# Kernel tuning notes

Measured on AMD Instinct MI355X. Metric: run time of the kernel, lower is better.

The kernel has to match this reference:

```python
import jax, jax.numpy as jnp
import numpy as np

N = 16        # state dim n
M = 8         # control dim m
T = 50        # time_steps
DT = 0.01     # delta_t
SQRT_DT = DT ** 0.5
GAMMA = 0.1
SIGMA = 0.2
TAU = 0.5
H = 10        # hidden width of subnets
BATCH = 32768


def _mlp(params, x):
    W1, b1, W2, b2, W3, b3 = params
    h = jnp.tanh(x @ W1 + b1)
    h = jnp.tanh(h @ W2 + b2)
    return h @ W3 + b3


def setup_inputs() -> dict:
    key = jax.random.key(0)
    ks = jax.random.split(key, 32)

    def dense(k, i, o):
        return (jax.random.normal(k, (i, o), jnp.float32) / np.float32(np.sqrt(i)))

    inp = {
        'dw': jax.random.normal(ks[0], (T, BATCH, 1), jnp.float32) * SQRT_DT,
        'X0': jax.random.uniform(ks[1], (BATCH, N), jnp.float32),
        'A': dense(ks[2], N, N),
        'Bmat': dense(ks[3], N, M),
        'Cmat': dense(ks[4], N, N),
        'Dmat': dense(ks[5], N, M),
        # phi: (n+1) -> 10 -> 10 -> m
        'phi_W1': dense(ks[6], N + 1, H), 'phi_b1': jnp.zeros((H,), jnp.float32),
        'phi_W2': dense(ks[7], H, H),     'phi_b2': jnp.zeros((H,), jnp.float32),
        'phi_W3': dense(ks[8], H, M),     'phi_b3': jnp.zeros((M,), jnp.float32),
        # Z: (n+1) -> 10 -> 10 -> n
        'Z_W1': dense(ks[9], N + 1, H),   'Z_b1': jnp.zeros((H,), jnp.float32),
        'Z_W2': dense(ks[10], H, H),      'Z_b2': jnp.zeros((H,), jnp.float32),
        'Z_W3': dense(ks[11], H, N),      'Z_b3': jnp.zeros((N,), jnp.float32),
        # Y0: n -> 10 -> 10 -> n
        'Y0_W1': dense(ks[12], N, H),     'Y0_b1': jnp.zeros((H,), jnp.float32),
        'Y0_W2': dense(ks[13], H, H),     'Y0_b2': jnp.zeros((H,), jnp.float32),
        'Y0_W3': dense(ks[14], H, N),     'Y0_b3': jnp.zeros((N,), jnp.float32),
    }
    return inp


def reference(dw, X0, A, Bmat, Cmat, Dmat,
              phi_W1, phi_b1, phi_W2, phi_b2, phi_W3, phi_b3,
              Z_W1, Z_b1, Z_W2, Z_b2, Z_W3, Z_b3,
              Y0_W1, Y0_b1, Y0_W2, Y0_b2, Y0_W3, Y0_b3):
    phi_p = (phi_W1, phi_b1, phi_W2, phi_b2, phi_W3, phi_b3)
    Z_p = (Z_W1, Z_b1, Z_W2, Z_b2, Z_W3, Z_b3)
    Y0_p = (Y0_W1, Y0_b1, Y0_W2, Y0_b2, Y0_W3, Y0_b3)

    B = X0.shape[0]
    Y = _mlp(Y0_p, X0)                              # [B, n]
    t_grid = jnp.arange(T, dtype=X0.dtype) * DT     # [T]
    w_trap = jnp.ones((T,), X0.dtype).at[1:-1].set(2.0)  # trapezoid weights

    def step(carry, xs):
        X, Yc, lc = carry
        dwi, t, w = xs                              # dwi: [B,1]
        state = jnp.concatenate(
            [jnp.broadcast_to(t, (B, 1)).astype(X.dtype), X], axis=1)  # [B, n+1]
        Zv = _mlp(Z_p, state)                       # [B, n]
        u = _mlp(phi_p, state)                      # [B, m] (project = identity)
        # b_mult(M, x) == x @ M.T
        drift_X = X @ A.T + u @ Bmat.T + GAMMA      # [B, n]
        diffusion_X = X @ Cmat.T + u @ Dmat.T + SIGMA
        drift_Y = -(Yc @ A + Zv @ Cmat + X)         # f_x(X,u) = X
        # stop_recording branch: gradient of dH / pre_phi
        dH = Yc @ Bmat + Zv @ Dmat + u              # f_u(X,u) = u -> [B, m]
        pre_phi = jax.lax.stop_gradient(u - TAU * dH)
        Xn = X + drift_X * DT + dwi * diffusion_X
        Yn = Yc + drift_Y * DT + dwi * Zv
        lc = lc + 0.5 * DT * w * jnp.sum(jnp.square(u - pre_phi), axis=1)
        return (Xn, Yn, lc), None

    init = (X0, Y, jnp.zeros((B,), X0.dtype))
    (X, Y, loss_control), _ = jax.lax.scan(step, init, (dw, t_grid, w_trap))
    loss_bsde = jnp.sum(jnp.square(Y - X), axis=1)  # g_x(X) = X
    return jnp.stack([jnp.mean(loss_bsde), jnp.mean(loss_control)])
```

## Files before the change

kernel.cpp:

```cpp
#include <hip/hip_runtime.h>

namespace {

typedef float v4f __attribute__((ext_vector_type(4)));
typedef _Float16 half4 __attribute__((ext_vector_type(4)));
typedef __fp16 fp16x2 __attribute__((ext_vector_type(2)));
typedef unsigned int uint32;

constexpr int   kB     = 32768;
constexpr int   kT     = 50;
constexpr float kDT    = 0.01f;
constexpr float kGamma = 0.1f;
constexpr float kSigma = 0.2f;
constexpr float kTau   = 0.5f;
constexpr float kA     = 2.8853900817779268f;

constexpr int kNFrag      = 17;
constexpr int kFragDwords = kNFrag * 128;
constexpr int kBiasFloats = 11 * 16;

__device__ __forceinline__ float fexp2(float x) {
#if __has_builtin(__builtin_amdgcn_exp2f)
  return __builtin_amdgcn_exp2f(x);
#else
  return exp2f(x);
#endif
}

__device__ __forceinline__ float fact(float x) {
  return __builtin_amdgcn_rcpf(fexp2(x) + 1.0f);
}

__device__ __forceinline__ v4f act4(v4f a) {
  v4f r;
  r[0] = fact(a[0]); r[1] = fact(a[1]);
  r[2] = fact(a[2]); r[3] = fact(a[3]);
  return r;
}

__device__ __forceinline__ uint32 pk2rtn(float a, float b) {
  union { _Float16 h[2]; uint32 u; } z;
  z.h[0] = (_Float16)a; z.h[1] = (_Float16)b;
  return z.u;
}

__global__ __launch_bounds__(64) void prep_kernel(
    const float* __restrict__ A,   const float* __restrict__ Bm,
    const float* __restrict__ Cm,  const float* __restrict__ Dm,
    const float* __restrict__ pW1, const float* __restrict__ pb1,
    const float* __restrict__ pW2, const float* __restrict__ pb2,
    const float* __restrict__ pW3, const float* __restrict__ pb3,
    const float* __restrict__ zW1, const float* __restrict__ zb1,
    const float* __restrict__ zW2, const float* __restrict__ zb2,
    const float* __restrict__ zW3, const float* __restrict__ zb3,
    const float* __restrict__ yW1, const float* __restrict__ yb1,
    const float* __restrict__ yW2, const float* __restrict__ yb2,
    const float* __restrict__ yW3, const float* __restrict__ yb3,
    uint32* __restrict__ ws)
{
  const int tid = threadIdx.x;
  const int blk = blockIdx.x;

  auto sum10 = [](const float* W, int stride, int mm) {
    float s = 0.f;
#pragma unroll
    for (int j = 0; j < 10; ++j) s += W[j * stride + mm];
    return s;
  };

  if (blk < kNFrag) {
    const int m = tid & 15, q = tid >> 4;
    const int p = blk;

    auto wv = [&](int k) -> float {
      switch (p) {
        case 0:  return (m < 10) ? kA * yW1[k * 10 + m] : 0.f;
        case 1:  return (m < 10 && k < 10) ? -2.f * kA * yW2[k * 10 + m] : 0.f;
        case 2:  return (k < 10) ? -2.f * yW3[k * 16 + m] : 0.f;
        case 3:  return (m < 10) ? kA * zW1[(k + 1) * 10 + m] : 0.f;
        case 4:  return (m < 10) ? kA * pW1[(k + 1) * 10 + m] : 0.f;
        case 5:  return (m < 10 && k < 10) ? -2.f * kA * zW2[k * 10 + m] : 0.f;
        case 6:  return (m < 10 && k < 10) ? -2.f * kA * pW2[k * 10 + m] : 0.f;
        case 7:  return (k < 10) ? -2.f * zW3[k * 16 + m] : 0.f;
        case 8:  return (m < 8 && k < 10) ? -2.f * pW3[k * 8 + m] : 0.f;
        case 9:  return A[m * 16 + k];
        case 10: return (k < 8) ? Bm[m * 8 + k] : 0.f;
        case 11: return Cm[m * 16 + k];
        case 12: return (k < 8) ? Dm[m * 8 + k] : 0.f;
        case 13: return A[k * 16 + m];
        case 14: return Cm[k * 16 + m];
        case 15: return (m < 8) ? Bm[k * 8 + m] : 0.f;
        case 16: return (m < 8) ? Dm[k * 8 + m] : 0.f;
      }
      return 0.f;
    };

    const int k0 = 4 * q;
    ws[p * 128 + tid * 2]     = pk2rtn(wv(k0),     wv(k0 + 1));
    ws[p * 128 + tid * 2 + 1] = pk2rtn(wv(k0 + 2), wv(k0 + 3));
  } else {
    float* bsf = (float*)(ws + kFragDwords);
    auto bval = [&](int a, int mm) -> float {
      const bool m10 = mm < 10;
      switch (a) {
        case 0:  return m10 ? kA * yb1[mm] : 0.f;
        case 1:  return m10 ? kA * (yb2[mm] + sum10(yW2, 10, mm)) : 0.f;
        case 2:  return yb3[mm] + sum10(yW3, 16, mm);
        case 3:  return m10 ? kA * (zb2[mm] + sum10(zW2, 10, mm)) : 0.f;
        case 4:  return m10 ? kA * (pb2[mm] + sum10(pW2, 10, mm)) : 0.f;
        case 5:  return zb3[mm] + sum10(zW3, 16, mm);
        case 6:  return (mm < 8) ? pb3[mm] + sum10(pW3, 8, mm) : 0.f;
        case 7:  return m10 ? kA * zW1[mm] : 0.f;
        case 8:  return m10 ? kA * zb1[mm] : 0.f;
        case 9:  return m10 ? kA * pW1[mm] : 0.f;
        case 10: return m10 ? kA * pb1[mm] : 0.f;
      }
      return 0.f;
    };
    for (int j = tid; j < kBiasFloats; j += 64) {
      bsf[j] = bval(j >> 4, j & 15);
    }
  }
}

__global__ __launch_bounds__(128)
__attribute__((amdgpu_waves_per_eu(2, 4)))
void bsde_kernel(const float* __restrict__ dw, const float* __restrict__ X0,
                 const uint32* __restrict__ wsu, float* __restrict__ out)
{
  const int tid  = threadIdx.x;
  const int w    = tid >> 6;
  const int lane = tid & 63;
  const int col  = lane & 15;
  const int quad = lane >> 4;
  const int e    = blockIdx.x * 16 + col;
  const int bq   = quad * 4;

  __shared__ float sx[2][64][4];
  __shared__ float su[2][64][4];

  auto ldfrag = [&](int p) -> half4 {
    union { uint2 u; half4 h; } z;
    z.u = *(const uint2*)(wsu + p * 128 + lane * 2);
    return z.h;
  };
  const float* bsf = (const float*)(wsu + kFragDwords);

  const half4 aL1 = ldfrag(w ? 4 : 3);
  const half4 aL2 = ldfrag(w ? 6 : 5);
  const half4 aL3 = ldfrag(w ? 8 : 7);
  const half4 aE0 = ldfrag(w ? 9 : 13);
  const half4 aE1 = ldfrag(w ? 10 : 14);
  const half4 aE2 = ldfrag(w ? 11 : 15);
  const half4 aE3 = ldfrag(w ? 12 : 16);
  const v4f c2 = *(const v4f*)&bsf[(w ? 4 : 3) * 16 + bq];
  const v4f c3 = *(const v4f*)&bsf[(w ? 6 : 5) * 16 + bq];
  const v4f vt = *(const v4f*)&bsf[(w ? 9 : 7) * 16 + bq];
  const v4f vb = *(const v4f*)&bsf[(w ? 10 : 8) * 16 + bq];

  auto pk4 = [](v4f a) -> half4 {
    union { fp16x2 p[2]; half4 h; } z;
    z.p[0] = __builtin_amdgcn_cvt_pkrtz(a[0], a[1]);
    z.p[1] = __builtin_amdgcn_cvt_pkrtz(a[2], a[3]);
    return z.h;
  };
  auto mm4 = [](half4 a, half4 b, v4f c) -> v4f {
    return __builtin_amdgcn_mfma_f32_16x16x16f16(a, b, c, 0, 0, 0);
  };

  const v4f gam4  = {kGamma, kGamma, kGamma, kGamma};
  const v4f sig4  = {kSigma, kSigma, kSigma, kSigma};
  const v4f zero4 = {0.f, 0.f, 0.f, 0.f};

  v4f x4 = *(const v4f*)&X0[e * 16 + bq];
  half4 xB = pk4(x4);
  v4f y4 = zero4;
  if (w == 0) {
    const half4 a0 = ldfrag(0), a1 = ldfrag(1), a2 = ldfrag(2);
    const v4f cy1 = *(const v4f*)&bsf[0 * 16 + bq];
    const v4f cy2 = *(const v4f*)&bsf[1 * 16 + bq];
    const v4f cy3 = *(const v4f*)&bsf[2 * 16 + bq];
    v4f h = mm4(a0, xB, cy1);
    v4f g = mm4(a1, pk4(act4(h)), cy2);
    y4    = mm4(a2, pk4(act4(g)), cy3);
  }

  float dwv = dw[e];
  float lcp = 0.0f;
  int buf = 0;

#pragma unroll 1
  for (int t = 0; t < kT; ++t) {
    const float dwn = (t < kT - 1) ? dw[(t + 1) * kB + e] : 0.0f;
    const float tv  = (float)t * kDT;
    const float wt  = (t == 0 || t == kT - 1) ? 1.0f : 2.0f;

    v4f c1;
#pragma unroll
    for (int r = 0; r < 4; ++r) c1[r] = vb[r] + tv * vt[r];

    v4f h = mm4(aL1, xB, c1);
    v4f g = mm4(aL2, pk4(act4(h)), c2);
    v4f o = mm4(aL3, pk4(act4(g)), c3);
    half4 oB = pk4(o);

    half4 yB = pk4(y4);
    const half4 firstB = w ? xB : yB;
    const v4f cA = w ? gam4 : x4;
    const v4f cB = w ? sig4 : zero4;

    v4f s1 = mm4(aE0, firstB, cA);
    v4f p1 = mm4(aE1, oB, s1);
    v4f s2 = mm4(aE2, firstB, cB);
    v4f p2 = mm4(aE3, oB, s2);

    v4f Xn, Yn;
    if (w) {
      *(v4f*)&su[buf][lane][0] = o;
#pragma unroll
      for (int r = 0; r < 4; ++r) Xn[r] = x4[r] + kDT * p1[r] + dwv * p2[r];
      *(v4f*)&sx[buf][lane][0] = Xn;
    } else {
#pragma unroll
      for (int r = 0; r < 4; ++r) Yn[r] = y4[r] - kDT * p1[r] + dwv * o[r];
    }

    __syncthreads();

    if (w) {
      x4 = Xn;
      xB = pk4(x4);
    } else {
      const v4f uu = *(const v4f*)&su[buf][lane][0];
      float ss = 0.0f;
#pragma unroll
      for (int r = 0; r < 4; ++r) { float d = p2[r] + uu[r]; ss += d * d; }
      lcp += (0.5f * kDT * kTau * kTau) * wt * ss;
      y4 = Yn;
      x4 = *(const v4f*)&sx[buf][lane][0];
      xB = pk4(x4);
    }
    dwv = dwn;
    buf ^= 1;
  }

  if (w == 0) {
    float bp = 0.0f;
#pragma unroll
    for (int r = 0; r < 4; ++r) { float d = y4[r] - x4[r]; bp += d * d; }
#pragma unroll
    for (int s = 32; s > 0; s >>= 1) {
      bp  += __shfl_down(bp,  s, 64);
      lcp += __shfl_down(lcp, s, 64);
    }
    if (lane == 0) {
      atomicAdd(&out[0], bp  * (1.0f / (float)kB));
      atomicAdd(&out[1], lcp * (1.0f / (float)kB));
    }
  }
}

}

extern "C" void kernel_launch(void* const* d_in, const int* in_sizes, int n_in,
                              void* d_out, int out_size, void* d_ws, size_t ws_size,
                              hipStream_t stream) {
  (void)in_sizes; (void)n_in; (void)ws_size; (void)out_size;

  const float* dw  = (const float*)d_in[0];
  const float* X0  = (const float*)d_in[1];
  const float* A   = (const float*)d_in[2];
  const float* Bm  = (const float*)d_in[3];
  const float* Cm  = (const float*)d_in[4];
  const float* Dm  = (const float*)d_in[5];
  const float* pW1 = (const float*)d_in[6];
  const float* pb1 = (const float*)d_in[7];
  const float* pW2 = (const float*)d_in[8];
  const float* pb2 = (const float*)d_in[9];
  const float* pW3 = (const float*)d_in[10];
  const float* pb3 = (const float*)d_in[11];
  const float* zW1 = (const float*)d_in[12];
  const float* zb1 = (const float*)d_in[13];
  const float* zW2 = (const float*)d_in[14];
  const float* zb2 = (const float*)d_in[15];
  const float* zW3 = (const float*)d_in[16];
  const float* zb3 = (const float*)d_in[17];
  const float* yW1 = (const float*)d_in[18];
  const float* yb1 = (const float*)d_in[19];
  const float* yW2 = (const float*)d_in[20];
  const float* yb2 = (const float*)d_in[21];
  const float* yW3 = (const float*)d_in[22];
  const float* yb3 = (const float*)d_in[23];
  float* out = (float*)d_out;
  unsigned int* ws = (unsigned int*)d_ws;

  (void)hipMemsetAsync(out, 0, 2 * sizeof(float), stream);

  prep_kernel<<<kNFrag + 1, 64, 0, stream>>>(
      A, Bm, Cm, Dm,
      pW1, pb1, pW2, pb2, pW3, pb3,
      zW1, zb1, zW2, zb2, zW3, zb3,
      yW1, yb1, yW2, yb2, yW3, yb3, ws);

  bsde_kernel<<<kB / 16, 128, 0, stream>>>(dw, X0, ws, out);
}
```

Measured before the change: 185.4 us.

## Fold MLP output layer into coupling matrices and skew Y wave one step behind X

Precomputes B·W3, D·W3, W3·C and W3·D products in the prep kernel so the coupling MFMAs consume the last hidden activation directly, which removes the dependent output-layer step from the X/Y critical path. The Y wave now runs one time step behind the X wave, reading X and u from shared memory written in the previous iteration. The goal is for the two waves' MFMA chains to overlap instead of serialising on a barrier each step. This adds one extra loop iteration and changes rounding, since fused weights are quantised to fp16 once.

```diff
diff --git a/kernel.cpp b/kernel.cpp
--- a/kernel.cpp
+++ b/kernel.cpp
@@ -17,7 +17,7 @@
 
 constexpr int kNFrag      = 17;
 constexpr int kFragDwords = kNFrag * 128;
-constexpr int kBiasFloats = 11 * 16;
+constexpr int kBiasFloats = 15 * 16;
 
 __device__ __forceinline__ float fexp2(float x) {
 #if __has_builtin(__builtin_amdgcn_exp2f)
@@ -73,6 +73,7 @@
     const int p = blk;
 
     auto wv = [&](int k) -> float {
+      float s = 0.f;
       switch (p) {
         case 0:  return (m < 10) ? kA * yW1[k * 10 + m] : 0.f;
         case 1:  return (m < 10 && k < 10) ? -2.f * kA * yW2[k * 10 + m] : 0.f;
@@ -84,13 +85,29 @@
         case 7:  return (k < 10) ? -2.f * zW3[k * 16 + m] : 0.f;
         case 8:  return (m < 8 && k < 10) ? -2.f * pW3[k * 8 + m] : 0.f;
         case 9:  return A[m * 16 + k];
-        case 10: return (k < 8) ? Bm[m * 8 + k] : 0.f;
         case 11: return Cm[m * 16 + k];
-        case 12: return (k < 8) ? Dm[m * 8 + k] : 0.f;
         case 13: return A[k * 16 + m];
-        case 14: return Cm[k * 16 + m];
         case 15: return (m < 8) ? Bm[k * 8 + m] : 0.f;
-        case 16: return (m < 8) ? Dm[k * 8 + m] : 0.f;
+        case 10:
+          if (k >= 10) return 0.f;
+#pragma unroll
+          for (int qq = 0; qq < 8; ++qq) s += Bm[m * 8 + qq] * pW3[k * 8 + qq];
+          return -2.f * s;
+        case 12:
+          if (k >= 10) return 0.f;
+#pragma unroll
+          for (int qq = 0; qq < 8; ++qq) s += Dm[m * 8 + qq] * pW3[k * 8 + qq];
+          return -2.f * s;
+        case 14:
+          if (k >= 10) return 0.f;
+#pragma unroll
+          for (int kk = 0; kk < 16; ++kk) s += zW3[k * 16 + kk] * Cm[kk * 16 + m];
+          return -2.f * s;
+        case 16:
+          if (m >= 8 || k >= 10) return 0.f;
+#pragma unroll
+          for (int kk = 0; kk < 16; ++kk) s += zW3[k * 16 + kk] * Dm[kk * 8 + m];
+          return -2.f * s;
       }
       return 0.f;
     };
@@ -100,20 +117,40 @@
     ws[p * 128 + tid * 2 + 1] = pk2rtn(wv(k0 + 2), wv(k0 + 3));
   } else {
     float* bsf = (float*)(ws + kFragDwords);
+    auto b3p = [&](int q) { return pb3[q] + sum10(pW3, 8, q); };
+    auto b3z = [&](int k) { return zb3[k] + sum10(zW3, 16, k); };
     auto bval = [&](int a, int mm) -> float {
       const bool m10 = mm < 10;
+      float s = 0.f;
       switch (a) {
         case 0:  return m10 ? kA * yb1[mm] : 0.f;
         case 1:  return m10 ? kA * (yb2[mm] + sum10(yW2, 10, mm)) : 0.f;
         case 2:  return yb3[mm] + sum10(yW3, 16, mm);
         case 3:  return m10 ? kA * (zb2[mm] + sum10(zW2, 10, mm)) : 0.f;
         case 4:  return m10 ? kA * (pb2[mm] + sum10(pW2, 10, mm)) : 0.f;
-        case 5:  return zb3[mm] + sum10(zW3, 16, mm);
-        case 6:  return (mm < 8) ? pb3[mm] + sum10(pW3, 8, mm) : 0.f;
+        case 5:  return b3z(mm);
+        case 6:  return (mm < 8) ? b3p(mm) : 0.f;
         case 7:  return m10 ? kA * zW1[mm] : 0.f;
         case 8:  return m10 ? kA * zb1[mm] : 0.f;
         case 9:  return m10 ? kA * pW1[mm] : 0.f;
         case 10: return m10 ? kA * pb1[mm] : 0.f;
+        case 11:
+#pragma unroll
+          for (int q = 0; q < 8; ++q) s += Bm[mm * 8 + q] * b3p(q);
+          return s;
+        case 12:
+#pragma unroll
+          for (int q = 0; q < 8; ++q) s += Dm[mm * 8 + q] * b3p(q);
+          return s;
+        case 13:
+#pragma unroll
+          for (int k = 0; k < 16; ++k) s += Cm[k * 16 + mm] * b3z(k);
+          return s;
+        case 14:
+          if (mm >= 8) return 0.f;
+#pragma unroll
+          for (int k = 0; k < 16; ++k) s += Dm[k * 8 + mm] * b3z(k);
+          return s;
       }
       return 0.f;
     };
@@ -149,14 +186,24 @@
   const half4 aL1 = ldfrag(w ? 4 : 3);
   const half4 aL2 = ldfrag(w ? 6 : 5);
   const half4 aL3 = ldfrag(w ? 8 : 7);
-  const half4 aE0 = ldfrag(w ? 9 : 13);
-  const half4 aE1 = ldfrag(w ? 10 : 14);
+  const half4 aE1 = ldfrag(w ? 9 : 13);
   const half4 aE2 = ldfrag(w ? 11 : 15);
-  const half4 aE3 = ldfrag(w ? 12 : 16);
+  const half4 aW1 = ldfrag(w ? 10 : 14);
+  const half4 aW2 = ldfrag(w ? 12 : 16);
   const v4f c2 = *(const v4f*)&bsf[(w ? 4 : 3) * 16 + bq];
   const v4f c3 = *(const v4f*)&bsf[(w ? 6 : 5) * 16 + bq];
   const v4f vt = *(const v4f*)&bsf[(w ? 9 : 7) * 16 + bq];
   const v4f vb = *(const v4f*)&bsf[(w ? 10 : 8) * 16 + bq];
+  v4f s1c, s2c;
+  {
+    const v4f ba = *(const v4f*)&bsf[(w ? 11 : 13) * 16 + bq];
+    const v4f bb = *(const v4f*)&bsf[(w ? 12 : 14) * 16 + bq];
+#pragma unroll
+    for (int r = 0; r < 4; ++r) {
+      s1c[r] = w ? (kGamma + ba[r]) : ba[r];
+      s2c[r] = w ? (kSigma + bb[r]) : bb[r];
+    }
+  }
 
   auto pk4 = [](v4f a) -> half4 {
     union { fp16x2 p[2]; half4 h; } z;
@@ -168,13 +215,10 @@
     return __builtin_amdgcn_mfma_f32_16x16x16f16(a, b, c, 0, 0, 0);
   };
 
-  const v4f gam4  = {kGamma, kGamma, kGamma, kGamma};
-  const v4f sig4  = {kSigma, kSigma, kSigma, kSigma};
-  const v4f zero4 = {0.f, 0.f, 0.f, 0.f};
-
   v4f x4 = *(const v4f*)&X0[e * 16 + bq];
   half4 xB = pk4(x4);
-  v4f y4 = zero4;
+  v4f y4 = {0.f, 0.f, 0.f, 0.f};
+  half4 yB = pk4(y4);
   if (w == 0) {
     const half4 a0 = ldfrag(0), a1 = ldfrag(1), a2 = ldfrag(2);
     const v4f cy1 = *(const v4f*)&bsf[0 * 16 + bq];
@@ -183,65 +227,78 @@
     v4f h = mm4(a0, xB, cy1);
     v4f g = mm4(a1, pk4(act4(h)), cy2);
     y4    = mm4(a2, pk4(act4(g)), cy3);
-  }
-
-  float dwv = dw[e];
+    yB    = pk4(y4);
+  }
+
+  float dwc = dw[e];
   float lcp = 0.0f;
-  int buf = 0;
 
 #pragma unroll 1
-  for (int t = 0; t < kT; ++t) {
-    const float dwn = (t < kT - 1) ? dw[(t + 1) * kB + e] : 0.0f;
-    const float tv  = (float)t * kDT;
-    const float wt  = (t == 0 || t == kT - 1) ? 1.0f : 2.0f;
-
-    v4f c1;
-#pragma unroll
-    for (int r = 0; r < 4; ++r) c1[r] = vb[r] + tv * vt[r];
-
-    v4f h = mm4(aL1, xB, c1);
-    v4f g = mm4(aL2, pk4(act4(h)), c2);
-    v4f o = mm4(aL3, pk4(act4(g)), c3);
-    half4 oB = pk4(o);
-
-    half4 yB = pk4(y4);
-    const half4 firstB = w ? xB : yB;
-    const v4f cA = w ? gam4 : x4;
-    const v4f cB = w ? sig4 : zero4;
-
-    v4f s1 = mm4(aE0, firstB, cA);
-    v4f p1 = mm4(aE1, oB, s1);
-    v4f s2 = mm4(aE2, firstB, cB);
-    v4f p2 = mm4(aE3, oB, s2);
-
-    v4f Xn, Yn;
+  for (int i = 0; i <= kT; ++i) {
+    const int idx = w ? (i + 1) : i;
+    const float dwn = (idx < kT) ? dw[idx * kB + e] : 0.0f;
+
     if (w) {
-      *(v4f*)&su[buf][lane][0] = o;
-#pragma unroll
-      for (int r = 0; r < 4; ++r) Xn[r] = x4[r] + kDT * p1[r] + dwv * p2[r];
-      *(v4f*)&sx[buf][lane][0] = Xn;
+      if (i < kT) {
+        const float tv = (float)i * kDT;
+        v4f c1;
+#pragma unroll
+        for (int r = 0; r < 4; ++r) c1[r] = vb[r] + tv * vt[r];
+        v4f h = mm4(aL1, xB, c1);
+        half4 hB = pk4(act4(h));
+        v4f g = mm4(aL2, hB, c2);
+        half4 gB = pk4(act4(g));
+        v4f u = mm4(aL3, gB, c3);
+        *(v4f*)&su[i & 1][lane][0] = u;
+        v4f s1 = mm4(aE1, xB, s1c);
+        v4f s2 = mm4(aE2, xB, s2c);
+        v4f dx = mm4(aW1, gB, s1);
+        v4f fx = mm4(aW2, gB, s2);
+        v4f Xn;
+#pragma unroll
+        for (int r = 0; r < 4; ++r) Xn[r] = x4[r] + kDT * dx[r] + dwc * fx[r];
+        *(v4f*)&sx[i & 1][lane][0] = Xn;
+        x4 = Xn;
+        xB = pk4(x4);
+      }
     } else {
-#pragma unroll
-      for (int r = 0; r < 4; ++r) Yn[r] = y4[r] - kDT * p1[r] + dwv * o[r];
-    }
-
+      if (i >= 1) {
+        const int s = i - 1;
+        const float tv = (float)s * kDT;
+        const float wt = (s == 0 || s == kT - 1) ? 1.0f : 2.0f;
+        v4f c1;
+#pragma unroll
+        for (int r = 0; r < 4; ++r) c1[r] = vb[r] + tv * vt[r];
+        v4f h = mm4(aL1, xB, c1);
+        half4 hB = pk4(act4(h));
+        v4f g = mm4(aL2, hB, c2);
+        half4 gB = pk4(act4(g));
+        v4f zv = mm4(aL3, gB, c3);
+        v4f s1yc;
+#pragma unroll
+        for (int r = 0; r < 4; ++r) s1yc[r] = x4[r] + s1c[r];
+        v4f s1y = mm4(aE1, yB, s1yc);
+        v4f s2y = mm4(aE2, yB, s2c);
+        v4f dy = mm4(aW1, gB, s1y);
+        v4f dh = mm4(aW2, gB, s2y);
+        const v4f uu = *(const v4f*)&su[s & 1][lane][0];
+        v4f Yn;
+        float ss = 0.0f;
+#pragma unroll
+        for (int r = 0; r < 4; ++r) {
+          Yn[r] = y4[r] - kDT * dy[r] + dwc * zv[r];
+          float d = dh[r] + uu[r];
+          ss += d * d;
+        }
+        lcp += (0.5f * kDT * kTau * kTau) * wt * ss;
+        y4 = Yn;
+        yB = pk4(y4);
+        x4 = *(const v4f*)&sx[s & 1][lane][0];
+        xB = pk4(x4);
+      }
+    }
     __syncthreads();
-
-    if (w) {
-      x4 = Xn;
-      xB = pk4(x4);
-    } else {
-      const v4f uu = *(const v4f*)&su[buf][lane][0];
-      float ss = 0.0f;
-#pragma unroll
-      for (int r = 0; r < 4; ++r) { float d = p2[r] + uu[r]; ss += d * d; }
-      lcp += (0.5f * kDT * kTau * kTau) * wt * ss;
-      y4 = Yn;
-      x4 = *(const v4f*)&sx[buf][lane][0];
-      xB = pk4(x4);
-    }
-    dwv = dwn;
-    buf ^= 1;
+    dwc = dwn;
   }
 
   if (w == 0) {
```

Measured after the change: 185.9 us (median of 3 runs). No clear change (+0.2%).
